# Kernel tuning notes

Measured on AMD Instinct MI355X. Metric: run time of the kernel, lower is better.

The kernel has to match this reference:

```python
import jax, jax.numpy as jnp
import numpy as np

NUM_HEADS = 16
HIDDEN = 1024
HEAD_DIM = HIDDEN // NUM_HEADS


def setup_inputs() -> dict:
    key = jax.random.key(0)
    ks = jax.random.split(key, 8)
    B, S = 4, 1024
    scale = 0.02
    return {
        "hidden_states": jax.random.normal(ks[0], (B, S, HIDDEN), jnp.float32),
        "attention_mask": jnp.zeros((B, 1, 1, S), jnp.float32),
        "Wq": jax.random.normal(ks[1], (HIDDEN, HIDDEN), jnp.float32) * scale,
        "bq": jnp.zeros((HIDDEN,), jnp.float32),
        "Wk": jax.random.normal(ks[2], (HIDDEN, HIDDEN), jnp.float32) * scale,
        "bk": jnp.zeros((HIDDEN,), jnp.float32),
        "Wv": jax.random.normal(ks[3], (HIDDEN, HIDDEN), jnp.float32) * scale,
        "bv": jnp.zeros((HIDDEN,), jnp.float32),
    }


def _split_heads(x):
    # [B,S,H] -> [B,heads,S,head_dim]
    B, S, _ = x.shape
    return x.reshape(B, S, NUM_HEADS, HEAD_DIM).transpose(0, 2, 1, 3)


def reference(hidden_states, attention_mask, Wq, bq, Wk, bk, Wv, bv):
    # torch.nn.Linear convention: y = x @ W.T + b
    q = _split_heads(hidden_states @ Wq.T + bq)
    k = _split_heads(hidden_states @ Wk.T + bk)
    v = _split_heads(hidden_states @ Wv.T + bv)
    scores = jnp.einsum('bhqd,bhkd->bhqk', q, k) * (HEAD_DIM ** -0.5)
    scores = scores + attention_mask  # broadcast [B,1,1,S]
    probs = jax.nn.softmax(scores, axis=-1)
    context = jnp.einsum('bhqk,bhkd->bhqd', probs, v)  # [B,heads,S,head_dim]
    B, _, S, _ = context.shape
    return context.transpose(0, 2, 1, 3).reshape(B, S, HIDDEN)
```

## Files before the change

### kernel.cpp

```cpp
#include <hip/hip_runtime.h>
#include <hip/hip_bf16.h>
#include <stdint.h>

#define NH 16
#define HID 1024
#define HD 64
#define NB 4
#define SS 1024
#define MTOT (NB*SS)

typedef __attribute__((ext_vector_type(8))) short bf16x8;
typedef __attribute__((ext_vector_type(4))) float f32x4;

__device__ __forceinline__ unsigned short f2bf(float f) {
  union { float f; unsigned u; } v; v.f = f;
  unsigned u = v.u;
  return (unsigned short)((u + 0x7FFFu + ((u >> 16) & 1u)) >> 16);
}

__device__ __forceinline__ unsigned pack2(float lo, float hi) {
  return (unsigned)f2bf(lo) | ((unsigned)f2bf(hi) << 16);
}

__device__ __forceinline__ void async16(void* lds, const void* g) {
  __builtin_amdgcn_global_load_lds(
      (const __attribute__((address_space(1))) unsigned*)g,
      (__attribute__((address_space(3))) unsigned*)lds, 16, 0, 0);
}

__global__ void cvt_all(const float4* __restrict__ X,
                        const float4* __restrict__ Wq,
                        const float4* __restrict__ Wk,
                        const float4* __restrict__ Wv,
                        ushort4* __restrict__ Xb,
                        ushort4* __restrict__ Wb) {
  int i = blockIdx.x * 256 + threadIdx.x;
  const float4* src; ushort4* dst; int idx;
  if (i < (MTOT * HID / 4)) {
    src = X; dst = Xb; idx = i;
  } else {
    int j = i - (MTOT * HID / 4);
    int sel = j >> 18;
    idx = j & 262143;
    src = (sel == 0) ? Wq : (sel == 1) ? Wk : Wv;
    dst = Wb + (size_t)sel * 262144;
  }
  float4 v = src[idx];
  ushort4 o;
  o.x = f2bf(v.x); o.y = f2bf(v.y); o.z = f2bf(v.z); o.w = f2bf(v.w);
  dst[idx] = o;
}

__global__ __launch_bounds__(256) void qkv_gemm(
    const ushort* __restrict__ Xb,
    const ushort* __restrict__ Wb,
    const float* __restrict__ bq,
    const float* __restrict__ bk,
    const float* __restrict__ bv,
    ushort* __restrict__ Q,
    ushort* __restrict__ K,
    ushort* __restrict__ Vt)
{
  __shared__ ushort Al[128 * 64];
  __shared__ ushort Bl[128 * 64];

  int bid = blockIdx.x;
  int swz = (bid & 7) * 96 + (bid >> 3);
  const int nbn = 3072 / 128;
  int bm = swz / nbn, bn = swz % nbn;
  int m0 = bm * 128, n0 = bn * 128;

  int tid = threadIdx.x;
  int wave = tid >> 6, lane = tid & 63;
  int g = lane >> 4, c = lane & 15;
  int wr = wave >> 1, wc = wave & 1;

  const ushort* Asrc = Xb + (size_t)(m0 + (tid >> 3)) * 1024 + (tid & 7) * 8;
  const ushort* Bsrc = Wb + (size_t)(n0 + (tid >> 3)) * 1024 + (tid & 7) * 8;

  f32x4 acc[4][4] = {};

  for (int ks = 0; ks < 16; ++ks) {
    int k0 = ks * 64;
    __syncthreads();
    #pragma unroll
    for (int i = 0; i < 4; ++i) {
      async16((char*)Al + i * 4096 + wave * 1024, Asrc + (size_t)i * 32 * 1024 + k0);
      async16((char*)Bl + i * 4096 + wave * 1024, Bsrc + (size_t)i * 32 * 1024 + k0);
    }
    __syncthreads();
    #pragma unroll
    for (int kk = 0; kk < 2; ++kk) {
      bf16x8 a[4], b[4];
      #pragma unroll
      for (int m = 0; m < 4; ++m)
        a[m] = *(const bf16x8*)((const char*)Al + (wr * 64 + m * 16 + c) * 128 + kk * 64 + g * 16);
      #pragma unroll
      for (int n = 0; n < 4; ++n)
        b[n] = *(const bf16x8*)((const char*)Bl + (wc * 64 + n * 16 + c) * 128 + kk * 64 + g * 16);
      #pragma unroll
      for (int m = 0; m < 4; ++m)
        #pragma unroll
        for (int n = 0; n < 4; ++n)
          acc[m][n] = __builtin_amdgcn_mfma_f32_16x16x32_bf16(a[m], b[n], acc[m][n], 0, 0, 0);
    }
  }

  int sel = n0 >> 10;
  const float* bp = (sel == 0) ? bq : (sel == 1) ? bk : bv;
  float scl = (sel == 0) ? 0.125f : 1.0f;

  #pragma unroll
  for (int n = 0; n < 4; ++n) {
    int nn = (n0 & 1023) + wc * 64 + n * 16 + c;
    float bias = bp[nn];
    int h = nn >> 6, d = nn & 63;
    #pragma unroll
    for (int m = 0; m < 4; ++m) {
      int rowg = m0 + wr * 64 + m * 16 + g * 4;
      int bb = rowg >> 10;
      int s = rowg & 1023;
      #pragma unroll
      for (int r = 0; r < 4; ++r) {
        float val = (acc[m][n][r] + bias) * scl;
        unsigned short ob = f2bf(val);
        if (sel == 0)
          Q[(size_t)((bb * 16 + h) * 1024 + s + r) * 64 + d] = ob;
        else if (sel == 1)
          K[(size_t)((bb * 16 + h) * 1024 + s + r) * 64 + d] = ob;
        else
          Vt[(size_t)((bb * 16 + h) * 64 + d) * 1024 + s + r] = ob;
      }
    }
  }
}

__global__ __launch_bounds__(256) void attn(
    const ushort* __restrict__ Q,
    const ushort* __restrict__ K,
    const ushort* __restrict__ Vt,
    const float* __restrict__ mask,
    float* __restrict__ out)
{
  __shared__ float mask_s[SS];
  __shared__ __attribute__((aligned(16))) char kv_lds[2][16384];

  int blk = blockIdx.x;
  int xcd = blk & 7;
  int j = blk >> 3;
  int bh = xcd * 8 + (j >> 4);
  int qt = j & 15;
  int b = bh >> 4, h = bh & 15;
  int tid = threadIdx.x, wave = tid >> 6, lane = tid & 63;
  int g = lane >> 4, c = lane & 15;
  int q0 = qt * 64 + wave * 16;

  for (int i = tid; i < SS; i += 256) mask_s[i] = mask[b * SS + i];
  __syncthreads();

  const ushort* Qb = Q + (size_t)bh * SS * 64;
  const ushort* Kb = K + (size_t)bh * SS * 64;
  const ushort* Vb = Vt + (size_t)bh * 64 * SS;

  bf16x8 qf0 = *(const bf16x8*)(Qb + (q0 + c) * 64 + g * 8);
  bf16x8 qf1 = *(const bf16x8*)(Qb + (q0 + c) * 64 + 32 + g * 8);

  int srow = lane >> 3;
  int schunk = lane & 7;
  const ushort* sptr[4];
  int soff[4];
  #pragma unroll
  for (int j2 = 0; j2 < 4; ++j2) {
    soff[j2] = wave * 4096 + j2 * 1024;
    if (wave < 2) {
      int row = wave * 32 + j2 * 8 + srow;
      sptr[j2] = Kb + (size_t)row * 64 + ((schunk ^ srow) << 3);
    } else {
      int d = (wave - 2) * 32 + j2 * 8 + srow;
      sptr[j2] = Vb + (size_t)d * SS + ((schunk ^ srow) << 3);
    }
  }
  const int sstep = (wave < 2) ? 64 * 64 : 64;

#define STAGE(bufidx) do {                              \
    char* lb_ = kv_lds[bufidx];                         \
    async16(lb_ + soff[0], sptr[0]);                    \
    async16(lb_ + soff[1], sptr[1]);                    \
    async16(lb_ + soff[2], sptr[2]);                    \
    async16(lb_ + soff[3], sptr[3]);                    \
    sptr[0] += sstep; sptr[1] += sstep;                 \
    sptr[2] += sstep; sptr[3] += sstep;                 \
  } while (0)

  f32x4 o[4] = {};
  float mrow = 0.f, lrow = 0.f;

  int addrA = ((((g & 1) << 1) + 0) * 16 + c) << 2;
  int addrB = ((((g & 1) << 1) + 1) * 16 + c) << 2;
  bool hiSel = (g >= 2);

  int cswz = c & 7;

  STAGE(0);

  for (int it = 0; it < 16; ++it) {
    int cur = it & 1;
    if (it < 15) {
      STAGE(cur ^ 1);
      asm volatile("s_waitcnt vmcnt(4)" ::: "memory");
    } else {
      asm volatile("s_waitcnt vmcnt(0)" ::: "memory");
    }
    __builtin_amdgcn_sched_barrier(0);
    __builtin_amdgcn_s_barrier();
    __builtin_amdgcn_sched_barrier(0);

    const char* kb0 = kv_lds[cur];
    const char* vb0 = kv_lds[cur] + 8192;

    f32x4 s[4];
    __builtin_amdgcn_s_setprio(1);
    #pragma unroll
    for (int t = 0; t < 4; ++t) {
      f32x4 z = {0.f, 0.f, 0.f, 0.f};
      bf16x8 ka = *(const bf16x8*)(kb0 + (t * 16 + c) * 128 + ((g ^ cswz) << 4));
      bf16x8 kB = *(const bf16x8*)(kb0 + (t * 16 + c) * 128 + (((4 + g) ^ cswz) << 4));
      z = __builtin_amdgcn_mfma_f32_16x16x32_bf16(ka, qf0, z, 0, 0, 0);
      z = __builtin_amdgcn_mfma_f32_16x16x32_bf16(kB, qf1, z, 0, 0, 0);
      s[t] = z;
    }
    __builtin_amdgcn_s_setprio(0);

    #pragma unroll
    for (int t = 0; t < 4; ++t) {
      f32x4 mk = *(const f32x4*)(&mask_s[it * 64 + t * 16 + g * 4]);
      s[t] += mk;
    }
    float mx = s[0][0];
    #pragma unroll
    for (int t = 0; t < 4; ++t)
      #pragma unroll
      for (int r = 0; r < 4; ++r) mx = fmaxf(mx, s[t][r]);
    mx = fmaxf(mx, __shfl_xor(mx, 16));
    mx = fmaxf(mx, __shfl_xor(mx, 32));

    if (!__all(mx <= mrow + 8.f)) {
      float mn = fmaxf(mrow, mx);
      float sc = __expf(mrow - mn);
      mrow = mn;
      lrow *= sc;
      #pragma unroll
      for (int r = 0; r < 4; ++r) {
        float scq = __shfl(sc, g * 4 + r);
        #pragma unroll
        for (int c4 = 0; c4 < 4; ++c4) o[c4][r] *= scq;
      }
    }

    f32x4 p[4];
    float rs = 0.f;
    #pragma unroll
    for (int t = 0; t < 4; ++t)
      #pragma unroll
      for (int r = 0; r < 4; ++r) {
        float e = __expf(s[t][r] - mrow);
        p[t][r] = e;
        rs += e;
      }
    rs += __shfl_xor(rs, 16);
    rs += __shfl_xor(rs, 32);
    lrow += rs;

    #pragma unroll
    for (int hh = 0; hh < 2; ++hh) {
      unsigned W0 = pack2(p[2 * hh][0], p[2 * hh][1]);
      unsigned W1 = pack2(p[2 * hh][2], p[2 * hh][3]);
      unsigned W2 = pack2(p[2 * hh + 1][0], p[2 * hh + 1][1]);
      unsigned W3 = pack2(p[2 * hh + 1][2], p[2 * hh + 1][3]);
      int w0l = __builtin_amdgcn_ds_bpermute(addrA, (int)W0);
      int w0h = __builtin_amdgcn_ds_bpermute(addrA, (int)W2);
      int w1l = __builtin_amdgcn_ds_bpermute(addrA, (int)W1);
      int w1h = __builtin_amdgcn_ds_bpermute(addrA, (int)W3);
      int w2l = __builtin_amdgcn_ds_bpermute(addrB, (int)W0);
      int w2h = __builtin_amdgcn_ds_bpermute(addrB, (int)W2);
      int w3l = __builtin_amdgcn_ds_bpermute(addrB, (int)W1);
      int w3h = __builtin_amdgcn_ds_bpermute(addrB, (int)W3);
      union { unsigned u[4]; bf16x8 v; } aw;
      aw.u[0] = (unsigned)(hiSel ? w0h : w0l);
      aw.u[1] = (unsigned)(hiSel ? w1h : w1l);
      aw.u[2] = (unsigned)(hiSel ? w2h : w2l);
      aw.u[3] = (unsigned)(hiSel ? w3h : w3l);
      bf16x8 pf = aw.v;
      __builtin_amdgcn_s_setprio(1);
      #pragma unroll
      for (int c4 = 0; c4 < 4; ++c4) {
        bf16x8 vf = *(const bf16x8*)(vb0 + (c4 * 16 + c) * 128 + (((hh * 4 + g) ^ cswz) << 4));
        o[c4] = __builtin_amdgcn_mfma_f32_16x16x32_bf16(pf, vf, o[c4], 0, 0, 0);
      }
      __builtin_amdgcn_s_setprio(0);
    }

    __builtin_amdgcn_sched_barrier(0);
    __builtin_amdgcn_s_barrier();
  }
#undef STAGE

  float lr[4];
  #pragma unroll
  for (int r = 0; r < 4; ++r)
    lr[r] = 1.0f / __shfl(lrow, g * 4 + r);

  #pragma unroll
  for (int c4 = 0; c4 < 4; ++c4) {
    #pragma unroll
    for (int r = 0; r < 4; ++r) {
      out[(size_t)(b * SS + q0 + g * 4 + r) * 1024 + h * 64 + c4 * 16 + c] =
          o[c4][r] * lr[r];
    }
  }
}

extern "C" void kernel_launch(void* const* d_in, const int* in_sizes, int n_in,
                              void* d_out, int out_size, void* d_ws, size_t ws_size,
                              hipStream_t stream) {
  const float* hs   = (const float*)d_in[0];
  const float* mask = (const float*)d_in[1];
  const float* Wq   = (const float*)d_in[2];
  const float* bq   = (const float*)d_in[3];
  const float* Wk   = (const float*)d_in[4];
  const float* bk   = (const float*)d_in[5];
  const float* Wv   = (const float*)d_in[6];
  const float* bv   = (const float*)d_in[7];
  float* out = (float*)d_out;

  char* ws = (char*)d_ws;
  ushort* Xb = (ushort*)(ws);
  ushort* Wb = (ushort*)(ws + (8u  << 20));
  ushort* Qp = (ushort*)(ws + (14u << 20));
  ushort* Kp = (ushort*)(ws + (22u << 20));
  ushort* Vt = (ushort*)(ws + (30u << 20));

  cvt_all<<<7168, 256, 0, stream>>>((const float4*)hs, (const float4*)Wq,
                                    (const float4*)Wk, (const float4*)Wv,
                                    (ushort4*)Xb, (ushort4*)Wb);
  qkv_gemm<<<768, 256, 0, stream>>>(Xb, Wb, bq, bk, bv, Qp, Kp, Vt);
  attn<<<1024, 256, 0, stream>>>(Qp, Kp, Vt, mask, out);
}
```

Baseline: 98.91 us.

## Switch attention to 32x32x16 MFMA with 32 query rows per wave and exp2 softmax

```diff
diff --git a/kernel.cpp b/kernel.cpp
--- a/kernel.cpp
+++ b/kernel.cpp
@@ -11,6 +11,9 @@
 
 typedef __attribute__((ext_vector_type(8))) short bf16x8;
 typedef __attribute__((ext_vector_type(4))) float f32x4;
+typedef __attribute__((ext_vector_type(16))) float f32x16;
+
+#define LOG2E 1.44269504088896f
 
 __device__ __forceinline__ unsigned short f2bf(float f) {
   union { float f; unsigned u; } v; v.f = f;
@@ -18,8 +21,20 @@
   return (unsigned short)((u + 0x7FFFu + ((u >> 16) & 1u)) >> 16);
 }
 
-__device__ __forceinline__ unsigned pack2(float lo, float hi) {
-  return (unsigned)f2bf(lo) | ((unsigned)f2bf(hi) << 16);
+__device__ __forceinline__ unsigned cvtpk(float lo, float hi) {
+  unsigned r;
+  asm("v_cvt_pk_bf16_f32 %0, %1, %2" : "=v"(r) : "v"(lo), "v"(hi));
+  return r;
+}
+
+__device__ __forceinline__ void pl32swap(unsigned &a, unsigned &b) {
+  asm("v_permlane32_swap_b32 %0, %1" : "+v"(a), "+v"(b));
+}
+
+__device__ __forceinline__ float exp2fast(float x) {
+  float r;
+  asm("v_exp_f32 %0, %1" : "=v"(r) : "v"(x));
+  return r;
 }
 
 __device__ __forceinline__ void async16(void* lds, const void* g) {
@@ -108,7 +123,7 @@
 
   int sel = n0 >> 10;
   const float* bp = (sel == 0) ? bq : (sel == 1) ? bk : bv;
-  float scl = (sel == 0) ? 0.125f : 1.0f;
+  float scl = (sel == 0) ? 0.125f * LOG2E : 1.0f;
 
   #pragma unroll
   for (int n = 0; n < 4; ++n) {
@@ -135,6 +150,25 @@
   }
 }
 
+__device__ __forceinline__ void build_pa(const f32x16& p, bf16x8& pa0, bf16x8& pa1) {
+  unsigned W0 = cvtpk(p[0],  p[1]);
+  unsigned W1 = cvtpk(p[2],  p[3]);
+  unsigned W2 = cvtpk(p[4],  p[5]);
+  unsigned W3 = cvtpk(p[6],  p[7]);
+  unsigned W4 = cvtpk(p[8],  p[9]);
+  unsigned W5 = cvtpk(p[10], p[11]);
+  unsigned W6 = cvtpk(p[12], p[13]);
+  unsigned W7 = cvtpk(p[14], p[15]);
+  pl32swap(W0, W2);
+  pl32swap(W1, W3);
+  pl32swap(W4, W6);
+  pl32swap(W5, W7);
+  union { unsigned u[4]; bf16x8 v; } a0, a1;
+  a0.u[0] = W0; a0.u[1] = W1; a0.u[2] = W2; a0.u[3] = W3;
+  a1.u[0] = W4; a1.u[1] = W5; a1.u[2] = W6; a1.u[3] = W7;
+  pa0 = a0.v; pa1 = a1.v;
+}
+
 __global__ __launch_bounds__(256) void attn(
     const ushort* __restrict__ Q,
     const ushort* __restrict__ K,
@@ -142,28 +176,29 @@
     const float* __restrict__ mask,
     float* __restrict__ out)
 {
-  __shared__ float mask_s[SS];
   __shared__ __attribute__((aligned(16))) char kv_lds[2][16384];
 
   int blk = blockIdx.x;
   int xcd = blk & 7;
   int j = blk >> 3;
-  int bh = xcd * 8 + (j >> 4);
-  int qt = j & 15;
+  int bh = xcd * 8 + (j >> 3);
+  int qt = j & 7;
   int b = bh >> 4, h = bh & 15;
   int tid = threadIdx.x, wave = tid >> 6, lane = tid & 63;
-  int g = lane >> 4, c = lane & 15;
-  int q0 = qt * 64 + wave * 16;
-
-  for (int i = tid; i < SS; i += 256) mask_s[i] = mask[b * SS + i];
-  __syncthreads();
+  int r31 = lane & 31, hi = lane >> 5;
+  int rsw = r31 & 7;
+  int hib = hi << 4;
+  int q0 = qt * 128 + wave * 32;
 
   const ushort* Qb = Q + (size_t)bh * SS * 64;
   const ushort* Kb = K + (size_t)bh * SS * 64;
   const ushort* Vb = Vt + (size_t)bh * 64 * SS;
-
-  bf16x8 qf0 = *(const bf16x8*)(Qb + (q0 + c) * 64 + g * 8);
-  bf16x8 qf1 = *(const bf16x8*)(Qb + (q0 + c) * 64 + 32 + g * 8);
+  const float* mb = mask + b * SS;
+
+  bf16x8 qf[4];
+  #pragma unroll
+  for (int kp = 0; kp < 4; ++kp)
+    qf[kp] = *(const bf16x8*)(Qb + (size_t)(q0 + r31) * 64 + kp * 16 + hi * 8);
 
   int srow = lane >> 3;
   int schunk = lane & 7;
@@ -192,14 +227,8 @@
     sptr[2] += sstep; sptr[3] += sstep;                 \
   } while (0)
 
-  f32x4 o[4] = {};
+  f32x16 o0 = (f32x16)0.0f, o1 = (f32x16)0.0f;
   float mrow = 0.f, lrow = 0.f;
-
-  int addrA = ((((g & 1) << 1) + 0) * 16 + c) << 2;
-  int addrB = ((((g & 1) << 1) + 1) * 16 + c) << 2;
-  bool hiSel = (g >= 2);
-
-  int cswz = c & 7;
 
   STAGE(0);
 
@@ -218,84 +247,74 @@
     const char* kb0 = kv_lds[cur];
     const char* vb0 = kv_lds[cur] + 8192;
 
-    f32x4 s[4];
+    f32x16 s0 = (f32x16)0.0f, s1 = (f32x16)0.0f;
     __builtin_amdgcn_s_setprio(1);
     #pragma unroll
-    for (int t = 0; t < 4; ++t) {
-      f32x4 z = {0.f, 0.f, 0.f, 0.f};
-      bf16x8 ka = *(const bf16x8*)(kb0 + (t * 16 + c) * 128 + ((g ^ cswz) << 4));
-      bf16x8 kB = *(const bf16x8*)(kb0 + (t * 16 + c) * 128 + (((4 + g) ^ cswz) << 4));
-      z = __builtin_amdgcn_mfma_f32_16x16x32_bf16(ka, qf0, z, 0, 0, 0);
-      z = __builtin_amdgcn_mfma_f32_16x16x32_bf16(kB, qf1, z, 0, 0, 0);
-      s[t] = z;
+    for (int kp = 0; kp < 4; ++kp) {
+      int ch = (((kp << 1) | hi) ^ rsw) << 4;
+      bf16x8 ka = *(const bf16x8*)(kb0 + r31 * 128 + ch);
+      bf16x8 kc = *(const bf16x8*)(kb0 + (32 + r31) * 128 + ch);
+      s0 = __builtin_amdgcn_mfma_f32_32x32x16_bf16(ka, qf[kp], s0, 0, 0, 0);
+      s1 = __builtin_amdgcn_mfma_f32_32x32x16_bf16(kc, qf[kp], s1, 0, 0, 0);
     }
     __builtin_amdgcn_s_setprio(0);
 
-    #pragma unroll
-    for (int t = 0; t < 4; ++t) {
-      f32x4 mk = *(const f32x4*)(&mask_s[it * 64 + t * 16 + g * 4]);
-      s[t] += mk;
-    }
-    float mx = s[0][0];
-    #pragma unroll
-    for (int t = 0; t < 4; ++t)
-      #pragma unroll
-      for (int r = 0; r < 4; ++r) mx = fmaxf(mx, s[t][r]);
-    mx = fmaxf(mx, __shfl_xor(mx, 16));
+    int kv = it * 64;
+    #pragma unroll
+    for (int sq = 0; sq < 4; ++sq) {
+      f32x4 mk0 = *(const f32x4*)(mb + kv + sq * 8 + hi * 4);
+      f32x4 mk1 = *(const f32x4*)(mb + kv + 32 + sq * 8 + hi * 4);
+      #pragma unroll
+      for (int r = 0; r < 4; ++r) {
+        s0[sq * 4 + r] = fmaf(mk0[r], LOG2E, s0[sq * 4 + r]);
+        s1[sq * 4 + r] = fmaf(mk1[r], LOG2E, s1[sq * 4 + r]);
+      }
+    }
+
+    float mx = s0[0];
+    #pragma unroll
+    for (int i = 1; i < 16; ++i) mx = fmaxf(mx, s0[i]);
+    #pragma unroll
+    for (int i = 0; i < 16; ++i) mx = fmaxf(mx, s1[i]);
     mx = fmaxf(mx, __shfl_xor(mx, 32));
 
-    if (!__all(mx <= mrow + 8.f)) {
+    if (!__all(mx <= mrow + 11.5416f)) {
       float mn = fmaxf(mrow, mx);
-      float sc = __expf(mrow - mn);
+      float sc = exp2fast(mrow - mn);
       mrow = mn;
       lrow *= sc;
       #pragma unroll
-      for (int r = 0; r < 4; ++r) {
-        float scq = __shfl(sc, g * 4 + r);
-        #pragma unroll
-        for (int c4 = 0; c4 < 4; ++c4) o[c4][r] *= scq;
+      for (int i = 0; i < 16; ++i) {
+        int qh = (i & 3) + 8 * (i >> 2);
+        float scq = __uint_as_float((unsigned)__builtin_amdgcn_ds_bpermute(
+            (qh << 2) + hib, (int)__float_as_uint(sc)));
+        o0[i] *= scq; o1[i] *= scq;
       }
     }
 
-    f32x4 p[4];
+    f32x16 p0, p1;
     float rs = 0.f;
     #pragma unroll
-    for (int t = 0; t < 4; ++t)
-      #pragma unroll
-      for (int r = 0; r < 4; ++r) {
-        float e = __expf(s[t][r] - mrow);
-        p[t][r] = e;
-        rs += e;
-      }
-    rs += __shfl_xor(rs, 16);
+    for (int i = 0; i < 16; ++i) { float e = exp2fast(s0[i] - mrow); p0[i] = e; rs += e; }
+    #pragma unroll
+    for (int i = 0; i < 16; ++i) { float e = exp2fast(s1[i] - mrow); p1[i] = e; rs += e; }
     rs += __shfl_xor(rs, 32);
     lrow += rs;
 
     #pragma unroll
-    for (int hh = 0; hh < 2; ++hh) {
-      unsigned W0 = pack2(p[2 * hh][0], p[2 * hh][1]);
-      unsigned W1 = pack2(p[2 * hh][2], p[2 * hh][3]);
-      unsigned W2 = pack2(p[2 * hh + 1][0], p[2 * hh + 1][1]);
-      unsigned W3 = pack2(p[2 * hh + 1][2], p[2 * hh + 1][3]);
-      int w0l = __builtin_amdgcn_ds_bpermute(addrA, (int)W0);
-      int w0h = __builtin_amdgcn_ds_bpermute(addrA, (int)W2);
-      int w1l = __builtin_amdgcn_ds_bpermute(addrA, (int)W1);
-      int w1h = __builtin_amdgcn_ds_bpermute(addrA, (int)W3);
-      int w2l = __builtin_amdgcn_ds_bpermute(addrB, (int)W0);
-      int w2h = __builtin_amdgcn_ds_bpermute(addrB, (int)W2);
-      int w3l = __builtin_amdgcn_ds_bpermute(addrB, (int)W1);
-      int w3h = __builtin_amdgcn_ds_bpermute(addrB, (int)W3);
-      union { unsigned u[4]; bf16x8 v; } aw;
-      aw.u[0] = (unsigned)(hiSel ? w0h : w0l);
-      aw.u[1] = (unsigned)(hiSel ? w1h : w1l);
-      aw.u[2] = (unsigned)(hiSel ? w2h : w2l);
-      aw.u[3] = (unsigned)(hiSel ? w3h : w3l);
-      bf16x8 pf = aw.v;
+    for (int T = 0; T < 2; ++T) {
+      bf16x8 pa0, pa1;
+      build_pa(T ? p1 : p0, pa0, pa1);
       __builtin_amdgcn_s_setprio(1);
       #pragma unroll
-      for (int c4 = 0; c4 < 4; ++c4) {
-        bf16x8 vf = *(const bf16x8*)(vb0 + (c4 * 16 + c) * 128 + (((hh * 4 + g) ^ cswz) << 4));
-        o[c4] = __builtin_amdgcn_mfma_f32_16x16x32_bf16(pf, vf, o[c4], 0, 0, 0);
+      for (int kh = 0; kh < 2; ++kh) {
+        int kap = 2 * T + kh;
+        int ch = (((kap << 1) | hi) ^ rsw) << 4;
+        bf16x8 va = *(const bf16x8*)(vb0 + r31 * 128 + ch);
+        bf16x8 vc = *(const bf16x8*)(vb0 + (32 + r31) * 128 + ch);
+        bf16x8 pf = kh ? pa1 : pa0;
+        o0 = __builtin_amdgcn_mfma_f32_32x32x16_bf16(pf, va, o0, 0, 0, 0);
+        o1 = __builtin_amdgcn_mfma_f32_32x32x16_bf16(pf, vc, o1, 0, 0, 0);
       }
       __builtin_amdgcn_s_setprio(0);
     }
@@ -305,18 +324,16 @@
   }
 #undef STAGE
 
-  float lr[4];
+  float inv = 1.0f / lrow;
   #pragma unroll
-  for (int r = 0; r < 4; ++r)
-    lr[r] = 1.0f / __shfl(lrow, g * 4 + r);
-
-  #pragma unroll
-  for (int c4 = 0; c4 < 4; ++c4) {
-    #pragma unroll
-    for (int r = 0; r < 4; ++r) {
-      out[(size_t)(b * SS + q0 + g * 4 + r) * 1024 + h * 64 + c4 * 16 + c] =
-          o[c4][r] * lr[r];
-    }
+  for (int i = 0; i < 16; ++i) {
+    int qh = (i & 3) + 8 * (i >> 2);
+    float li = __uint_as_float((unsigned)__builtin_amdgcn_ds_bpermute(
+        (qh << 2) + hib, (int)__float_as_uint(inv)));
+    int row = q0 + qh + 4 * hi;
+    float* op = out + (size_t)(b * SS + row) * 1024 + h * 64 + r31;
+    op[0]  = o0[i] * li;
+    op[32] = o1[i] * li;
   }
 }
 
@@ -344,5 +361,5 @@
                                     (const float4*)Wk, (const float4*)Wv,
                                     (ushort4*)Xb, (ushort4*)Wb);
   qkv_gemm<<<768, 256, 0, stream>>>(Xb, Wb, bq, bk, bv, Qp, Kp, Vt);
-  attn<<<1024, 256, 0, stream>>>(Qp, Kp, Vt, mask, out);
-}
+  attn<<<512, 256, 0, stream>>>(Qp, Kp, Vt, mask, out);
+}
```

Result: faster. 87.99 us (-11.0%).
